# Performance work log

Measured on AMD Instinct MI355X. Metric: run time of the kernel, lower is better.

Reference implementation:

```python
import jax, jax.numpy as jnp
import numpy as np

B, C, L = 16, 256, 16384
M = C // 4  # mid_channels = in_channels // ratio (reduction=True)
LN_EPS = 1e-5


def setup_inputs() -> dict:
    key = jax.random.key(0)
    ks = jax.random.split(key, 8)
    s = 0.05
    return {
        "x": jax.random.normal(ks[0], (B, C, L), dtype=jnp.float32),
        "w_mask": jax.random.normal(ks[1], (C,), dtype=jnp.float32) * s,   # conv_mask weight (1,C,1) squeezed
        "b_mask": jax.random.normal(ks[2], (), dtype=jnp.float32) * s,
        "w1": jax.random.normal(ks[3], (M, C), dtype=jnp.float32) * s,      # conv1x1 C->M
        "b1": jax.random.normal(ks[4], (M,), dtype=jnp.float32) * s,
        "ln_g": jnp.ones((M,), dtype=jnp.float32),                           # LayerNorm([M,1]) weight
        "ln_b": jnp.zeros((M,), dtype=jnp.float32),
        "w2": jax.random.normal(ks[5], (C, M), dtype=jnp.float32) * s,      # conv1x1 M->C
        "b2": jax.random.normal(ks[6], (C,), dtype=jnp.float32) * s,
    }


def reference(x, w_mask, b_mask, w1, b1, ln_g, ln_b, w2, b2):
    # spatial attention pooling: conv_mask (1x1 conv C->1) + softmax over seq_len
    logits = jnp.einsum("bcl,c->bl", x, w_mask) + b_mask          # (B, L)
    attn = jax.nn.softmax(logits, axis=-1)                         # (B, L)
    ctx = jnp.einsum("bcl,bl->bc", x, attn)                        # (B, C)  == matmul pooling

    # channel_add_conv: conv1x1 -> LayerNorm([M,1]) -> ReLU -> conv1x1
    h = jnp.einsum("bc,mc->bm", ctx, w1) + b1                      # (B, M)
    mu = jnp.mean(h, axis=-1, keepdims=True)
    var = jnp.mean((h - mu) ** 2, axis=-1, keepdims=True)
    h = (h - mu) * jax.lax.rsqrt(var + LN_EPS) * ln_g + ln_b
    h = jax.nn.relu(h)
    add = jnp.einsum("bm,cm->bc", h, w2) + b2                      # (B, C)

    return x + add[:, :, None]                                     # broadcast over seq_len
```

## Files before the change

kernel.cpp:

```cpp
#include <hip/hip_runtime.h>
#include <math.h>

#define Bn 16
#define Cn 256
#define Ln 16384
#define Mn 64
#define LN_EPS 1e-5f
#define CHUNK 32
#define NCH (Ln / CHUNK)
#define XSTR 33

typedef float v4f __attribute__((ext_vector_type(4)));

__global__ __launch_bounds__(256) void k_pool(
        const float* __restrict__ x, const float* __restrict__ w_mask,
        const float* __restrict__ b_mask,
        float* __restrict__ ctxU,
        float* __restrict__ mz) {
    const int ch = blockIdx.x, b = blockIdx.y;
    const int t = threadIdx.x;
    __shared__ float xs[Cn * XSTR];
    __shared__ float wm_s[Cn];
    __shared__ float red2[8 * CHUNK];
    __shared__ float e_s[CHUNK];

    wm_s[t] = w_mask[t];

    const size_t xbase = (size_t)b * Cn * Ln + (size_t)ch * CHUNK;
    const int c0 = t >> 3;
    const int f4 = t & 7;
    #pragma unroll
    for (int r = 0; r < 8; ++r) {
        const int c = r * 32 + c0;
        float4 v = *(const float4*)(x + xbase + (size_t)c * Ln + 4 * f4);
        float* dst = xs + c * XSTR + 4 * f4;
        dst[0] = v.x; dst[1] = v.y; dst[2] = v.z; dst[3] = v.w;
    }
    __syncthreads();

    const int hw = t >> 5, lA = t & 31;
    {
        float p = 0.f;
        #pragma unroll 8
        for (int k = 0; k < 32; ++k) {
            const int c = hw * 32 + k;
            p += xs[c * XSTR + lA] * wm_s[c];
        }
        red2[hw * CHUNK + lA] = p;
    }
    __syncthreads();
    if (t < CHUNK) {
        float logit = b_mask[0];
        #pragma unroll
        for (int j = 0; j < 8; ++j) logit += red2[j * CHUNK + t];
        float m = logit;
        for (int off = 16; off; off >>= 1) m = fmaxf(m, __shfl_xor(m, off, 32));
        const float e = expf(logit - m);
        e_s[t] = e;
        float z = e;
        for (int off = 16; off; off >>= 1) z += __shfl_xor(z, off, 32);
        if (t == 0) {
            mz[(b * NCH + ch) * 2 + 0] = m;
            mz[(b * NCH + ch) * 2 + 1] = z;
        }
    }
    __syncthreads();

    float acc = 0.f;
    #pragma unroll 8
    for (int l = 0; l < CHUNK; ++l)
        acc += xs[t * XSTR + l] * e_s[l];
    ctxU[((size_t)b * NCH + ch) * Cn + t] = acc;
}

__global__ void k_ctx(const float* __restrict__ ctxU, const float* __restrict__ mz,
                      float* __restrict__ ctx) {
    const int cblk = blockIdx.x, b = blockIdx.y;
    const int t = threadIdx.x;
    __shared__ float sc_s[NCH];
    __shared__ float red8[8];
    __shared__ float red[256];

    const float m0 = mz[(b * NCH + t) * 2],       z0 = mz[(b * NCH + t) * 2 + 1];
    const float m1 = mz[(b * NCH + 256 + t) * 2], z1 = mz[(b * NCH + 256 + t) * 2 + 1];
    float m = fmaxf(m0, m1);
    for (int off = 32; off; off >>= 1) m = fmaxf(m, __shfl_xor(m, off, 64));
    if ((t & 63) == 0) red8[t >> 6] = m;
    __syncthreads();
    const float M = fmaxf(fmaxf(red8[0], red8[1]), fmaxf(red8[2], red8[3]));
    float zw = z0 * expf(m0 - M) + z1 * expf(m1 - M);
    for (int off = 32; off; off >>= 1) zw += __shfl_xor(zw, off, 64);
    if ((t & 63) == 0) red8[4 + (t >> 6)] = zw;
    __syncthreads();
    const float Z = red8[4] + red8[5] + red8[6] + red8[7];
    sc_s[t]       = expf(m0 - M) / Z;
    sc_s[256 + t] = expf(m1 - M) / Z;
    __syncthreads();

    const int cl = t & 15, chl = t >> 4;
    const int c = cblk * 16 + cl;
    float p = 0.f;
    #pragma unroll 8
    for (int j = 0; j < 32; ++j) {
        const int chk = j * 16 + chl;
        p += ctxU[((size_t)b * NCH + chk) * Cn + c] * sc_s[chk];
    }
    red[chl * 16 + cl] = p;
    __syncthreads();
    if (t < 16) {
        float s = 0.f;
        #pragma unroll
        for (int j = 0; j < 16; ++j) s += red[j * 16 + t];
        ctx[b * Cn + cblk * 16 + t] = s;
    }
}

__global__ void k_mlp(const float* __restrict__ ctx, const float* __restrict__ w1,
                      const float* __restrict__ b1, const float* __restrict__ ln_g,
                      const float* __restrict__ ln_b, const float* __restrict__ w2,
                      const float* __restrict__ b2, float* __restrict__ add) {
    const int b = blockIdx.x;
    const int t = threadIdx.x;
    __shared__ float ctx_s[Cn];
    __shared__ float h_s[Mn];
    ctx_s[t] = ctx[b * Cn + t];
    __syncthreads();

    const int m4 = t >> 2, j = t & 3;
    float hp = 0.f;
    for (int c = j; c < Cn; c += 4) hp += ctx_s[c] * w1[m4 * Cn + c];
    hp += __shfl_xor(hp, 1, 64);
    hp += __shfl_xor(hp, 2, 64);
    if (j == 0) h_s[m4] = hp + b1[m4];
    __syncthreads();

    if (t < 64) {
        float h = h_s[t];
        float mu = h;
        for (int off = 32; off; off >>= 1) mu += __shfl_xor(mu, off, 64);
        mu *= (1.f / 64.f);
        const float d = h - mu;
        float var = d * d;
        for (int off = 32; off; off >>= 1) var += __shfl_xor(var, off, 64);
        var *= (1.f / 64.f);
        h = d * rsqrtf(var + LN_EPS) * ln_g[t] + ln_b[t];
        h_s[t] = fmaxf(h, 0.f);
    }
    __syncthreads();

    float a = b2[t];
    #pragma unroll
    for (int mm = 0; mm < Mn; ++mm) a += h_s[mm] * w2[t * Mn + mm];
    add[b * Cn + t] = a;
}

__global__ void k_out(const float* __restrict__ x, const float* __restrict__ add,
                      float* __restrict__ out) {
    const int flat = blockIdx.y * gridDim.x + blockIdx.x;
    const int rev  = (int)(gridDim.x * gridDim.y) - 1 - flat;
    const int bc   = rev >> 2;
    const int kblk = rev & 3;
    const float a = add[bc];
    const size_t base = (size_t)bc * Ln + (size_t)kblk * 4096;
    const float4* xi = (const float4*)(x + base);
    v4f* xo = (v4f*)(out + base);
    const int t = threadIdx.x;
    #pragma unroll
    for (int k = 0; k < 4; ++k) {
        float4 v = xi[k * 256 + t];
        v4f o = {v.x + a, v.y + a, v.z + a, v.w + a};
        __builtin_nontemporal_store(o, xo + k * 256 + t);
    }
}

extern "C" void kernel_launch(void* const* d_in, const int* in_sizes, int n_in,
                              void* d_out, int out_size, void* d_ws, size_t ws_size,
                              hipStream_t stream) {
    const float* x      = (const float*)d_in[0];
    const float* w_mask = (const float*)d_in[1];
    const float* b_mask = (const float*)d_in[2];
    const float* w1     = (const float*)d_in[3];
    const float* b1     = (const float*)d_in[4];
    const float* ln_g   = (const float*)d_in[5];
    const float* ln_b   = (const float*)d_in[6];
    const float* w2     = (const float*)d_in[7];
    const float* b2     = (const float*)d_in[8];
    float* out = (float*)d_out;

    float* ws   = (float*)d_ws;
    float* ctxU = ws;
    float* mz   = ctxU + (size_t)Bn * NCH * Cn;
    float* ctx  = mz + (size_t)Bn * NCH * 2;
    float* add  = ctx + (size_t)Bn * Cn;

    k_pool<<<dim3(NCH, Bn), 256, 0, stream>>>(x, w_mask, b_mask, ctxU, mz);
    k_ctx<<<dim3(Cn / 16, Bn), 256, 0, stream>>>(ctxU, mz, ctx);
    k_mlp<<<Bn, 256, 0, stream>>>(ctx, w1, b1, ln_g, ln_b, w2, b2, add);
    k_out<<<dim3(4, Bn * Cn), 256, 0, stream>>>(x, add, out);
}
```

Baseline: 142.7 us.

## Process eight chunks per pool block with online softmax and register prefetch

Each pooling block now walks eight 32-column chunks and merges them with a running max/sum (online softmax), prefetching the next chunk into registers while computing the current one. The logit dot product is folded into the load path using per-thread mask weights. This cuts partial-result writes and shrinks the k_ctx reduction from 512 to 64 partials per batch. It trades away parallelism, since the pool grid drops to 1024 blocks, and it adds register pressure from the double float4 buffers. It also drops the reversed block ordering in k_out, which previously made the output pass start on the most recently touched data for L2 reuse.

```diff
diff --git a/kernel.cpp b/kernel.cpp
--- a/kernel.cpp
+++ b/kernel.cpp
@@ -7,7 +7,8 @@
 #define Mn 64
 #define LN_EPS 1e-5f
 #define CHUNK 32
-#define NCH (Ln / CHUNK)
+#define NSUB 8
+#define NCHB (Ln / (CHUNK * NSUB))
 #define XSTR 33
 
 typedef float v4f __attribute__((ext_vector_type(4)));
@@ -17,95 +18,113 @@
         const float* __restrict__ b_mask,
         float* __restrict__ ctxU,
         float* __restrict__ mz) {
-    const int ch = blockIdx.x, b = blockIdx.y;
-    const int t = threadIdx.x;
-    __shared__ float xs[Cn * XSTR];
+    const int blk = blockIdx.x, b = blockIdx.y;
+    const int t = threadIdx.x;
+    const int c0 = t >> 3, f4 = t & 7;
+    __shared__ float xs[2][Cn * XSTR];
     __shared__ float wm_s[Cn];
-    __shared__ float red2[8 * CHUNK];
+    __shared__ float redA[32 * 32];
     __shared__ float e_s[CHUNK];
+    __shared__ float mzs[2];
 
     wm_s[t] = w_mask[t];
 
-    const size_t xbase = (size_t)b * Cn * Ln + (size_t)ch * CHUNK;
-    const int c0 = t >> 3;
-    const int f4 = t & 7;
-    #pragma unroll
-    for (int r = 0; r < 8; ++r) {
-        const int c = r * 32 + c0;
-        float4 v = *(const float4*)(x + xbase + (size_t)c * Ln + 4 * f4);
-        float* dst = xs + c * XSTR + 4 * f4;
-        dst[0] = v.x; dst[1] = v.y; dst[2] = v.z; dst[3] = v.w;
-    }
-    __syncthreads();
-
-    const int hw = t >> 5, lA = t & 31;
-    {
-        float p = 0.f;
+    const size_t xrow = (size_t)b * Cn * Ln + (size_t)blk * (CHUNK * NSUB);
+    const float* xc[8];
+    #pragma unroll
+    for (int r = 0; r < 8; ++r)
+        xc[r] = x + xrow + (size_t)(r * 32 + c0) * Ln + 4 * f4;
+
+    float4 r0[8], r1[8];
+    #pragma unroll
+    for (int r = 0; r < 8; ++r) r0[r] = *(const float4*)(xc[r]);
+    __syncthreads();
+    float wm_r[8];
+    #pragma unroll
+    for (int r = 0; r < 8; ++r) wm_r[r] = wm_s[r * 32 + c0];
+    const float bm = b_mask[0];
+
+    float acc = 0.f, m_run = -1e30f, z_run = 0.f;
+
+    #pragma unroll
+    for (int k = 0; k < NSUB; ++k) {
+        float4* cur = (k & 1) ? r1 : r0;
+        float4* nxt = (k & 1) ? r0 : r1;
+        if (k < NSUB - 1) {
+            #pragma unroll
+            for (int r = 0; r < 8; ++r)
+                nxt[r] = *(const float4*)(xc[r] + (k + 1) * CHUNK);
+        }
+        float4 p = {0.f, 0.f, 0.f, 0.f};
+        #pragma unroll
+        for (int r = 0; r < 8; ++r) {
+            float4 v = cur[r];
+            const float w = wm_r[r];
+            p.x += v.x * w; p.y += v.y * w; p.z += v.z * w; p.w += v.w * w;
+            float* dst = &xs[k & 1][(r * 32 + c0) * XSTR + 4 * f4];
+            dst[0] = v.x; dst[1] = v.y; dst[2] = v.z; dst[3] = v.w;
+        }
+        *(float4*)&redA[c0 * 32 + 4 * f4] = p;
+        __syncthreads();
+        if (t < 32) {
+            float logit = bm;
+            #pragma unroll 8
+            for (int i = 0; i < 32; ++i) logit += redA[i * 32 + t];
+            float mc = logit;
+            for (int off = 16; off; off >>= 1) mc = fmaxf(mc, __shfl_xor(mc, off, 32));
+            const float mn = fmaxf(m_run, mc);
+            const float e = expf(logit - mn);
+            e_s[t] = e;
+            float z = e;
+            for (int off = 16; off; off >>= 1) z += __shfl_xor(z, off, 32);
+            if (t == 0) { mzs[0] = mn; mzs[1] = z; }
+        }
+        __syncthreads();
+        const float mn = mzs[0], zc = mzs[1];
+        const float sa = expf(m_run - mn);
+        float s = 0.f;
         #pragma unroll 8
-        for (int k = 0; k < 32; ++k) {
-            const int c = hw * 32 + k;
-            p += xs[c * XSTR + lA] * wm_s[c];
-        }
-        red2[hw * CHUNK + lA] = p;
-    }
-    __syncthreads();
-    if (t < CHUNK) {
-        float logit = b_mask[0];
-        #pragma unroll
-        for (int j = 0; j < 8; ++j) logit += red2[j * CHUNK + t];
-        float m = logit;
-        for (int off = 16; off; off >>= 1) m = fmaxf(m, __shfl_xor(m, off, 32));
-        const float e = expf(logit - m);
-        e_s[t] = e;
-        float z = e;
-        for (int off = 16; off; off >>= 1) z += __shfl_xor(z, off, 32);
-        if (t == 0) {
-            mz[(b * NCH + ch) * 2 + 0] = m;
-            mz[(b * NCH + ch) * 2 + 1] = z;
-        }
-    }
-    __syncthreads();
-
-    float acc = 0.f;
-    #pragma unroll 8
-    for (int l = 0; l < CHUNK; ++l)
-        acc += xs[t * XSTR + l] * e_s[l];
-    ctxU[((size_t)b * NCH + ch) * Cn + t] = acc;
+        for (int l = 0; l < CHUNK; ++l)
+            s += xs[k & 1][t * XSTR + l] * e_s[l];
+        acc = acc * sa + s;
+        z_run = z_run * sa + zc;
+        m_run = mn;
+    }
+
+    ctxU[((size_t)b * NCHB + blk) * Cn + t] = acc;
+    if (t == 0) {
+        mz[(b * NCHB + blk) * 2 + 0] = m_run;
+        mz[(b * NCHB + blk) * 2 + 1] = z_run;
+    }
 }
 
 __global__ void k_ctx(const float* __restrict__ ctxU, const float* __restrict__ mz,
                       float* __restrict__ ctx) {
     const int cblk = blockIdx.x, b = blockIdx.y;
     const int t = threadIdx.x;
-    __shared__ float sc_s[NCH];
-    __shared__ float red8[8];
+    __shared__ float sc_s[NCHB];
     __shared__ float red[256];
 
-    const float m0 = mz[(b * NCH + t) * 2],       z0 = mz[(b * NCH + t) * 2 + 1];
-    const float m1 = mz[(b * NCH + 256 + t) * 2], z1 = mz[(b * NCH + 256 + t) * 2 + 1];
-    float m = fmaxf(m0, m1);
-    for (int off = 32; off; off >>= 1) m = fmaxf(m, __shfl_xor(m, off, 64));
-    if ((t & 63) == 0) red8[t >> 6] = m;
-    __syncthreads();
-    const float M = fmaxf(fmaxf(red8[0], red8[1]), fmaxf(red8[2], red8[3]));
-    float zw = z0 * expf(m0 - M) + z1 * expf(m1 - M);
-    for (int off = 32; off; off >>= 1) zw += __shfl_xor(zw, off, 64);
-    if ((t & 63) == 0) red8[4 + (t >> 6)] = zw;
-    __syncthreads();
-    const float Z = red8[4] + red8[5] + red8[6] + red8[7];
-    sc_s[t]       = expf(m0 - M) / Z;
-    sc_s[256 + t] = expf(m1 - M) / Z;
-    __syncthreads();
-
-    const int cl = t & 15, chl = t >> 4;
+    if (t < NCHB) {
+        const float mt = mz[(b * NCHB + t) * 2];
+        const float zt = mz[(b * NCHB + t) * 2 + 1];
+        float M = mt;
+        for (int off = 32; off; off >>= 1) M = fmaxf(M, __shfl_xor(M, off, 64));
+        float zw = zt * expf(mt - M);
+        for (int off = 32; off; off >>= 1) zw += __shfl_xor(zw, off, 64);
+        sc_s[t] = expf(mt - M) / zw;
+    }
+    __syncthreads();
+
+    const int cl = t & 15, g = t >> 4;
     const int c = cblk * 16 + cl;
     float p = 0.f;
-    #pragma unroll 8
-    for (int j = 0; j < 32; ++j) {
-        const int chk = j * 16 + chl;
-        p += ctxU[((size_t)b * NCH + chk) * Cn + c] * sc_s[chk];
-    }
-    red[chl * 16 + cl] = p;
+    #pragma unroll
+    for (int j = 0; j < 4; ++j) {
+        const int chk = g * 4 + j;
+        p += ctxU[((size_t)b * NCHB + chk) * Cn + c] * sc_s[chk];
+    }
+    red[g * 16 + cl] = p;
     __syncthreads();
     if (t < 16) {
         float s = 0.f;
@@ -156,12 +175,9 @@
 
 __global__ void k_out(const float* __restrict__ x, const float* __restrict__ add,
                       float* __restrict__ out) {
-    const int flat = blockIdx.y * gridDim.x + blockIdx.x;
-    const int rev  = (int)(gridDim.x * gridDim.y) - 1 - flat;
-    const int bc   = rev >> 2;
-    const int kblk = rev & 3;
+    const int bc = blockIdx.y;
     const float a = add[bc];
-    const size_t base = (size_t)bc * Ln + (size_t)kblk * 4096;
+    const size_t base = (size_t)bc * Ln + (size_t)blockIdx.x * 4096;
     const float4* xi = (const float4*)(x + base);
     v4f* xo = (v4f*)(out + base);
     const int t = threadIdx.x;
@@ -189,11 +205,11 @@
 
     float* ws   = (float*)d_ws;
     float* ctxU = ws;
-    float* mz   = ctxU + (size_t)Bn * NCH * Cn;
-    float* ctx  = mz + (size_t)Bn * NCH * 2;
+    float* mz   = ctxU + (size_t)Bn * NCHB * Cn;
+    float* ctx  = mz + (size_t)Bn * NCHB * 2;
     float* add  = ctx + (size_t)Bn * Cn;
 
-    k_pool<<<dim3(NCH, Bn), 256, 0, stream>>>(x, w_mask, b_mask, ctxU, mz);
+    k_pool<<<dim3(NCHB, Bn), 256, 0, stream>>>(x, w_mask, b_mask, ctxU, mz);
     k_ctx<<<dim3(Cn / 16, Bn), 256, 0, stream>>>(ctxU, mz, ctx);
     k_mlp<<<Bn, 256, 0, stream>>>(ctx, w1, b1, ln_g, ln_b, w2, b2, add);
     k_out<<<dim3(4, Bn * Cn), 256, 0, stream>>>(x, add, out);
```

Result: no change. 144.5 us (+1.3%).

## Fuse ctx combine and MLP into pool kernel via last-block atomic counter

Applied to the files above, without the earlier changes.

Folds the chunk-softmax combine and the MLP into the pooling kernel. A per-batch atomic counter lets the last finishing block do the reduction over all chunks and compute the add vector. This removes two kernel launches and the ctx round trip through global memory, at the cost of a memset launch and a serialized tail in which one block per batch reads 512x256 partials alone. The output kernel also drops its reversed block ordering, which may reduce L2 reuse of x left over from the pooling pass.

```diff
diff --git a/kernel.cpp b/kernel.cpp
--- a/kernel.cpp
+++ b/kernel.cpp
@@ -12,17 +12,22 @@
 
 typedef float v4f __attribute__((ext_vector_type(4)));
 
-__global__ __launch_bounds__(256) void k_pool(
+__global__ __launch_bounds__(256) void k_pool_fused(
         const float* __restrict__ x, const float* __restrict__ w_mask,
         const float* __restrict__ b_mask,
         float* __restrict__ ctxU,
-        float* __restrict__ mz) {
+        float* __restrict__ mz,
+        const float* __restrict__ w1, const float* __restrict__ b1,
+        const float* __restrict__ ln_g, const float* __restrict__ ln_b,
+        const float* __restrict__ w2, const float* __restrict__ b2,
+        float* __restrict__ add, int* __restrict__ cnt) {
     const int ch = blockIdx.x, b = blockIdx.y;
     const int t = threadIdx.x;
     __shared__ float xs[Cn * XSTR];
     __shared__ float wm_s[Cn];
     __shared__ float red2[8 * CHUNK];
     __shared__ float e_s[CHUNK];
+    __shared__ int last_s;
 
     wm_s[t] = w_mask[t];
 
@@ -71,15 +76,21 @@
     for (int l = 0; l < CHUNK; ++l)
         acc += xs[t * XSTR + l] * e_s[l];
     ctxU[((size_t)b * NCH + ch) * Cn + t] = acc;
-}
 
-__global__ void k_ctx(const float* __restrict__ ctxU, const float* __restrict__ mz,
-                      float* __restrict__ ctx) {
-    const int cblk = blockIdx.x, b = blockIdx.y;
-    const int t = threadIdx.x;
-    __shared__ float sc_s[NCH];
-    __shared__ float red8[8];
-    __shared__ float red[256];
+    __syncthreads();
+    if (t == 0) {
+        __threadfence();
+        last_s = (atomicAdd(&cnt[b], 1) == NCH - 1);
+    }
+    __syncthreads();
+    if (!last_s) return;
+    if (t == 0) __threadfence();
+    __syncthreads();
+
+    float* sc_s  = xs;
+    float* ctx_s = xs + 512;
+    float* h_s   = xs + 768;
+    float* red8  = xs + 832;
 
     const float m0 = mz[(b * NCH + t) * 2],       z0 = mz[(b * NCH + t) * 2 + 1];
     const float m1 = mz[(b * NCH + 256 + t) * 2], z1 = mz[(b * NCH + 256 + t) * 2 + 1];
@@ -97,33 +108,13 @@
     sc_s[256 + t] = expf(m1 - M) / Z;
     __syncthreads();
 
-    const int cl = t & 15, chl = t >> 4;
-    const int c = cblk * 16 + cl;
-    float p = 0.f;
-    #pragma unroll 8
-    for (int j = 0; j < 32; ++j) {
-        const int chk = j * 16 + chl;
-        p += ctxU[((size_t)b * NCH + chk) * Cn + c] * sc_s[chk];
+    {
+        float s = 0.f;
+        #pragma unroll 8
+        for (int chk = 0; chk < NCH; ++chk)
+            s += ctxU[((size_t)b * NCH + chk) * Cn + t] * sc_s[chk];
+        ctx_s[t] = s;
     }
-    red[chl * 16 + cl] = p;
-    __syncthreads();
-    if (t < 16) {
-        float s = 0.f;
-        #pragma unroll
-        for (int j = 0; j < 16; ++j) s += red[j * 16 + t];
-        ctx[b * Cn + cblk * 16 + t] = s;
-    }
-}
-
-__global__ void k_mlp(const float* __restrict__ ctx, const float* __restrict__ w1,
-                      const float* __restrict__ b1, const float* __restrict__ ln_g,
-                      const float* __restrict__ ln_b, const float* __restrict__ w2,
-                      const float* __restrict__ b2, float* __restrict__ add) {
-    const int b = blockIdx.x;
-    const int t = threadIdx.x;
-    __shared__ float ctx_s[Cn];
-    __shared__ float h_s[Mn];
-    ctx_s[t] = ctx[b * Cn + t];
     __syncthreads();
 
     const int m4 = t >> 2, j = t & 3;
@@ -156,12 +147,9 @@
 
 __global__ void k_out(const float* __restrict__ x, const float* __restrict__ add,
                       float* __restrict__ out) {
-    const int flat = blockIdx.y * gridDim.x + blockIdx.x;
-    const int rev  = (int)(gridDim.x * gridDim.y) - 1 - flat;
-    const int bc   = rev >> 2;
-    const int kblk = rev & 3;
+    const int bc = blockIdx.y;
     const float a = add[bc];
-    const size_t base = (size_t)bc * Ln + (size_t)kblk * 4096;
+    const size_t base = (size_t)bc * Ln + (size_t)blockIdx.x * 4096;
     const float4* xi = (const float4*)(x + base);
     v4f* xo = (v4f*)(out + base);
     const int t = threadIdx.x;
@@ -190,11 +178,12 @@
     float* ws   = (float*)d_ws;
     float* ctxU = ws;
     float* mz   = ctxU + (size_t)Bn * NCH * Cn;
-    float* ctx  = mz + (size_t)Bn * NCH * 2;
-    float* add  = ctx + (size_t)Bn * Cn;
+    float* add  = mz + (size_t)Bn * NCH * 2;
+    int*   cnt  = (int*)(add + (size_t)Bn * Cn);
 
-    k_pool<<<dim3(NCH, Bn), 256, 0, stream>>>(x, w_mask, b_mask, ctxU, mz);
-    k_ctx<<<dim3(Cn / 16, Bn), 256, 0, stream>>>(ctxU, mz, ctx);
-    k_mlp<<<Bn, 256, 0, stream>>>(ctx, w1, b1, ln_g, ln_b, w2, b2, add);
+    hipMemsetAsync(cnt, 0, Bn * sizeof(int), stream);
+    k_pool_fused<<<dim3(NCH, Bn), 256, 0, stream>>>(x, w_mask, b_mask, ctxU, mz,
+                                                    w1, b1, ln_g, ln_b, w2, b2,
+                                                    add, cnt);
     k_out<<<dim3(4, Bn * Cn), 256, 0, stream>>>(x, add, out);
 }
```

Result: slower. 472.4 us (+231.1%).
